# Optimization experiments

Measured on AMD Instinct MI355X. Metric: run time of the kernel, lower is better.

## Reference

```python
import jax, jax.numpy as jnp
import numpy as np

N_NODES = 200000
N_EDGES = 6400000
N_GRAPHS = 1000


def setup_inputs() -> dict:
    key = jax.random.key(0)
    ks = jax.random.split(key, 8)
    x = jax.random.normal(ks[0], (N_NODES, 2), dtype=jnp.float32)
    edge_index = jax.random.randint(ks[1], (2, N_EDGES), 0, N_NODES, dtype=jnp.int32)
    batch = jnp.sort(jax.random.randint(ks[2], (N_NODES,), 0, N_GRAPHS, dtype=jnp.int32))
    W1 = jax.random.normal(ks[3], (2, 16), dtype=jnp.float32) * (1.0 / np.sqrt(2))
    b1 = jnp.zeros((16,), jnp.float32)
    W2 = jax.random.normal(ks[4], (16, 32), dtype=jnp.float32) * (1.0 / np.sqrt(16))
    b2 = jnp.zeros((32,), jnp.float32)
    Wfc1 = jax.random.normal(ks[5], (32, 16), dtype=jnp.float32) * (1.0 / np.sqrt(32))
    bfc1 = jnp.zeros((16,), jnp.float32)
    Wfc2 = jax.random.normal(ks[6], (16, 1), dtype=jnp.float32) * (1.0 / np.sqrt(16))
    bfc2 = jnp.zeros((1,), jnp.float32)
    return {"x": x, "edge_index": edge_index, "batch": batch,
            "W1": W1, "b1": b1, "W2": W2, "b2": b2,
            "Wfc1": Wfc1, "bfc1": bfc1, "Wfc2": Wfc2, "bfc2": bfc2}


def _gcn_norm(edge_index, n_nodes):
    # PyG GCNConv default: add self loops, symmetric normalization.
    loops = jnp.arange(n_nodes, dtype=edge_index.dtype)
    src = jnp.concatenate([edge_index[0], loops])  # message source (row)
    dst = jnp.concatenate([edge_index[1], loops])  # aggregation target (col)
    deg = jax.ops.segment_sum(jnp.ones_like(dst, jnp.float32), dst, num_segments=n_nodes)
    dinv = jnp.where(deg > 0, jax.lax.rsqrt(jnp.maximum(deg, 1.0)), 0.0)
    norm = dinv[src] * dinv[dst]  # [E + N]
    return src, dst, norm


def _gcn_conv(h, W, b, src, dst, norm, n_nodes):
    h = h @ W                                      # transform first (small width)
    msg = h[src] * norm[:, None]                   # gather + scale: [E+N, F]
    out = jax.ops.segment_sum(msg, dst, num_segments=n_nodes)
    return out + b


def reference(x, edge_index, batch, W1, b1, W2, b2, Wfc1, bfc1, Wfc2, bfc2):
    n = x.shape[0]
    src, dst, norm = _gcn_norm(edge_index, n)
    h = jax.nn.relu(_gcn_conv(x, W1, b1, src, dst, norm, n))
    h = jax.nn.relu(_gcn_conv(h, W2, b2, src, dst, norm, n))
    # global_mean_pool over graph ids
    sums = jax.ops.segment_sum(h, batch, num_segments=N_GRAPHS)
    cnts = jax.ops.segment_sum(jnp.ones((n,), h.dtype), batch, num_segments=N_GRAPHS)
    pooled = sums / jnp.maximum(cnts, 1.0)[:, None]  # [G, 32]
    out = jax.nn.relu(pooled @ Wfc1 + bfc1)
    out = out @ Wfc2 + bfc2                          # [G, 1]
    return out.squeeze(-1)
```

## Files before the change

kernel.cpp:

```cpp
#include <hip/hip_runtime.h>
#include <hip/hip_fp16.h>

static inline size_t align256(size_t x) { return (x + 255) & ~size_t(255); }

#define CAP 36864

__global__ __launch_bounds__(512) void k_scatter(const int* __restrict__ ei,
                                                 int* __restrict__ bcursor,
                                                 unsigned* __restrict__ bdata, int E) {
    __shared__ int lcount[256];
    __shared__ int gbase[256];
    int t = threadIdx.x;
    if (t < 256) lcount[t] = 0;
    __syncthreads();
    int chunk = blockIdx.x * 8192;
    int srcv[16], bkt[16], rank[16], dl[16];
#pragma unroll
    for (int k = 0; k < 16; ++k) {
        int e = chunk + k * 512 + t;
        bkt[k] = -1;
        if (e < E) {
            int sv = ei[e], d = ei[E + e];
            int b = d >> 10;
            srcv[k] = sv; bkt[k] = b; dl[k] = d & 1023;
            rank[k] = atomicAdd(&lcount[b], 1);
        }
    }
    __syncthreads();
    if (t < 256) {
        int c = lcount[t];
        gbase[t] = t * CAP + (c ? atomicAdd(&bcursor[t], c) : 0);
    }
    __syncthreads();
#pragma unroll
    for (int k = 0; k < 16; ++k) {
        if (bkt[k] >= 0)
            bdata[gbase[bkt[k]] + rank[k]] = ((unsigned)dl[k] << 18) | (unsigned)srcv[k];
    }
}

__global__ void k_bscan2(const int* __restrict__ bcursor, int* __restrict__ bbase,
                         int NBv, int E) {
    __shared__ int lds[256];
    int t = threadIdx.x;
    int v = (t < NBv) ? bcursor[t] : 0;
    lds[t] = v;
    __syncthreads();
    for (int off = 1; off < 256; off <<= 1) {
        int x = (t >= off) ? lds[t - off] : 0;
        __syncthreads();
        lds[t] += x;
        __syncthreads();
    }
    if (t < NBv) bbase[t] = lds[t] - v;
    if (t == 0) bbase[NBv] = E;
}

__global__ __launch_bounds__(1024) void k_build(const unsigned* __restrict__ bdata,
                                                const int* __restrict__ bbase,
                                                int* __restrict__ row_ptr,
                                                float* __restrict__ dinv,
                                                int* __restrict__ col,
                                                const float* __restrict__ x,
                                                float2* __restrict__ xt,
                                                int N, int E, int NBv) {
    __shared__ int curs[1024];
    __shared__ int sums[256];
    __shared__ int stage[CAP];
    int* hist = stage;
    int bkt = blockIdx.x;
    int t = threadIdx.x;
    int tb = bbase[bkt];
    int count = bbase[bkt + 1] - tb;
    int fs = bkt * CAP;
    int node0 = bkt << 10;
    int nn = N - node0; if (nn > 1024) nn = 1024;
    hist[t] = 0;
    __syncthreads();
    for (int e = t; e < count; e += 1024)
        atomicAdd(&hist[bdata[fs + e] >> 18], 1);
    __syncthreads();
    int v0 = 0, v1 = 0, v2 = 0, v3 = 0, s = 0;
    if (t < 256) {
        int b4 = t * 4;
        v0 = hist[b4]; v1 = hist[b4 + 1]; v2 = hist[b4 + 2]; v3 = hist[b4 + 3];
        s = v0 + v1 + v2 + v3;
        sums[t] = s;
    }
    __syncthreads();
    for (int off = 1; off < 256; off <<= 1) {
        int xv = 0;
        if (t < 256 && t >= off) xv = sums[t - off];
        __syncthreads();
        if (t < 256) sums[t] += xv;
        __syncthreads();
    }
    if (t < 256) {
        int b4 = t * 4;
        int e0 = sums[t] - s;
        int e1 = e0 + v0, e2 = e1 + v1, e3 = e2 + v2;
        curs[b4] = e0; curs[b4 + 1] = e1; curs[b4 + 2] = e2; curs[b4 + 3] = e3;
        if (b4 < nn)     { row_ptr[node0 + b4]     = tb + e0; dinv[node0 + b4]     = rsqrtf((float)v0 + 1.f); }
        if (b4 + 1 < nn) { row_ptr[node0 + b4 + 1] = tb + e1; dinv[node0 + b4 + 1] = rsqrtf((float)v1 + 1.f); }
        if (b4 + 2 < nn) { row_ptr[node0 + b4 + 2] = tb + e2; dinv[node0 + b4 + 2] = rsqrtf((float)v2 + 1.f); }
        if (b4 + 3 < nn) { row_ptr[node0 + b4 + 3] = tb + e3; dinv[node0 + b4 + 3] = rsqrtf((float)v3 + 1.f); }
    }
    if (bkt == NBv - 1 && t == 0) row_ptr[N] = E;
    __syncthreads();
    for (int e = t; e < count; e += 1024) {
        unsigned p = bdata[fs + e];
        int dl = p >> 18;
        int pos = atomicAdd(&curs[dl], 1);
        stage[pos] = (int)(p & 0x3FFFFu);
    }
    __syncthreads();
    for (int i = t; i < count; i += 1024)
        col[tb + i] = stage[i];
    for (int i = t; i < nn; i += 1024) {
        int node = node0 + i;
        float d2 = dinv[node];
        xt[node] = make_float2(x[node * 2] * d2, x[node * 2 + 1] * d2);
    }
}

__global__ __launch_bounds__(256) void k_conv1_fused(const int* __restrict__ rp,
                                                     const int* __restrict__ col,
                                                     const float2* __restrict__ xt,
                                                     const float* __restrict__ dinv,
                                                     const float* __restrict__ W1,
                                                     const float* __restrict__ b1,
                                                     uint2* __restrict__ ht, int n) {
    int gt = blockIdx.x * 256 + threadIdx.x;
    int node = gt >> 2;
    int q = gt & 3;
    if (node >= n) return;
    int rs = rp[node], re = rp[node + 1];
    float a0 = 0.f, a1 = 0.f;
    int e = rs + q;
    for (; e + 12 < re; e += 16) {
        int c0 = __builtin_nontemporal_load(col + e);
        int c1 = __builtin_nontemporal_load(col + e + 4);
        int c2 = __builtin_nontemporal_load(col + e + 8);
        int c3 = __builtin_nontemporal_load(col + e + 12);
        float2 v0 = xt[c0];
        float2 v1 = xt[c1];
        float2 v2 = xt[c2];
        float2 v3 = xt[c3];
        a0 += (v0.x + v1.x) + (v2.x + v3.x);
        a1 += (v0.y + v1.y) + (v2.y + v3.y);
    }
    for (; e < re; e += 4) {
        float2 v = xt[__builtin_nontemporal_load(col + e)];
        a0 += v.x; a1 += v.y;
    }
    if (q == 0) { float2 sf = xt[node]; a0 += sf.x; a1 += sf.y; }
    a0 += __shfl_xor(a0, 1); a0 += __shfl_xor(a0, 2);
    a1 += __shfl_xor(a1, 1); a1 += __shfl_xor(a1, 2);
    float dv = dinv[node];
    a0 *= dv; a1 *= dv;
    int f0 = q * 4;
    float v0 = fmaxf(a0 * W1[f0]     + a1 * W1[16 + f0]     + b1[f0],     0.f) * dv;
    float v1 = fmaxf(a0 * W1[f0 + 1] + a1 * W1[16 + f0 + 1] + b1[f0 + 1], 0.f) * dv;
    float v2 = fmaxf(a0 * W1[f0 + 2] + a1 * W1[16 + f0 + 2] + b1[f0 + 2], 0.f) * dv;
    float v3 = fmaxf(a0 * W1[f0 + 3] + a1 * W1[16 + f0 + 3] + b1[f0 + 3], 0.f) * dv;
    __half2 h0 = __floats2half2_rn(v0, v1);
    __half2 h1 = __floats2half2_rn(v2, v3);
    uint2 w;
    w.x = *reinterpret_cast<unsigned*>(&h0);
    w.y = *reinterpret_cast<unsigned*>(&h1);
    ht[(size_t)node * 4 + q] = w;
}

__global__ __launch_bounds__(256) void k_gather2(const int* __restrict__ rp,
                                                 const int* __restrict__ col,
                                                 const uint4* __restrict__ ht,
                                                 const float* __restrict__ dinv,
                                                 float* __restrict__ agg, int N) {
    int gt = blockIdx.x * 256 + threadIdx.x;
    int node = gt >> 1;
    int hf = gt & 1;
    if (node >= N) return;
    int rs = rp[node], re = rp[node + 1];
    const uint4* __restrict__ base = ht + hf;
    float s0 = 0.f, s1 = 0.f, s2 = 0.f, s3 = 0.f, s4 = 0.f, s5 = 0.f, s6 = 0.f, s7 = 0.f;
    int e = rs;
    for (; e + 8 <= re; e += 8) {
        int c[8];
#pragma unroll
        for (int k = 0; k < 8; ++k) c[k] = __builtin_nontemporal_load(col + e + k);
        uint4 u[8];
#pragma unroll
        for (int k = 0; k < 8; ++k) u[k] = base[(size_t)c[k] * 2];
#pragma unroll
        for (int k = 0; k < 8; ++k) {
            float2 f0 = __half22float2(*reinterpret_cast<__half2*>(&u[k].x));
            float2 f1 = __half22float2(*reinterpret_cast<__half2*>(&u[k].y));
            float2 f2 = __half22float2(*reinterpret_cast<__half2*>(&u[k].z));
            float2 f3 = __half22float2(*reinterpret_cast<__half2*>(&u[k].w));
            s0 += f0.x; s1 += f0.y; s2 += f1.x; s3 += f1.y;
            s4 += f2.x; s5 += f2.y; s6 += f3.x; s7 += f3.y;
        }
    }
    for (; e < re; ++e) {
        uint4 u = base[(size_t)__builtin_nontemporal_load(col + e) * 2];
        float2 f0 = __half22float2(*reinterpret_cast<__half2*>(&u.x));
        float2 f1 = __half22float2(*reinterpret_cast<__half2*>(&u.y));
        float2 f2 = __half22float2(*reinterpret_cast<__half2*>(&u.z));
        float2 f3 = __half22float2(*reinterpret_cast<__half2*>(&u.w));
        s0 += f0.x; s1 += f0.y; s2 += f1.x; s3 += f1.y;
        s4 += f2.x; s5 += f2.y; s6 += f3.x; s7 += f3.y;
    }
    {
        uint4 u = base[(size_t)node * 2];
        float2 f0 = __half22float2(*reinterpret_cast<__half2*>(&u.x));
        float2 f1 = __half22float2(*reinterpret_cast<__half2*>(&u.y));
        float2 f2 = __half22float2(*reinterpret_cast<__half2*>(&u.z));
        float2 f3 = __half22float2(*reinterpret_cast<__half2*>(&u.w));
        s0 += f0.x; s1 += f0.y; s2 += f1.x; s3 += f1.y;
        s4 += f2.x; s5 += f2.y; s6 += f3.x; s7 += f3.y;
    }
    float dv = dinv[node];
    float* dst = agg + (size_t)node * 16 + hf * 8;
    __builtin_nontemporal_store(s0 * dv, dst);
    __builtin_nontemporal_store(s1 * dv, dst + 1);
    __builtin_nontemporal_store(s2 * dv, dst + 2);
    __builtin_nontemporal_store(s3 * dv, dst + 3);
    __builtin_nontemporal_store(s4 * dv, dst + 4);
    __builtin_nontemporal_store(s5 * dv, dst + 5);
    __builtin_nontemporal_store(s6 * dv, dst + 6);
    __builtin_nontemporal_store(s7 * dv, dst + 7);
}

__global__ __launch_bounds__(256) void k_trans_pool(const float* __restrict__ agg,
                                                    const float* __restrict__ W2,
                                                    const float* __restrict__ b2,
                                                    const int* __restrict__ batch,
                                                    float* __restrict__ gsum, int N) {
    __shared__ float aggs[64][17];
    __shared__ float h2s[64][33];
    __shared__ float w2s[512];
    __shared__ float b2s[32];
    __shared__ int   bids[64];
    int t = threadIdx.x;
    if (t < 128) ((float4*)w2s)[t] = ((const float4*)W2)[t];
    if (t < 32)  b2s[t] = b2[t];
    int node0 = blockIdx.x * 64;
    if (t < 64)  bids[t] = (node0 + t < N) ? batch[node0 + t] : -1;
    {
        int nl = t >> 2, q = t & 3;
        int node = node0 + nl;
        float4 v = make_float4(0.f, 0.f, 0.f, 0.f);
        if (node < N) v = *(const float4*)(agg + (size_t)node * 16 + (size_t)q * 4);
        int c0 = q * 4;
        aggs[nl][c0] = v.x; aggs[nl][c0 + 1] = v.y;
        aggs[nl][c0 + 2] = v.z; aggs[nl][c0 + 3] = v.w;
    }
    __syncthreads();
    {
        int nl = t >> 2;
        int jq = (t & 3) * 8;
        float o[8];
#pragma unroll
        for (int j = 0; j < 8; ++j) o[j] = b2s[jq + j];
#pragma unroll
        for (int k = 0; k < 16; ++k) {
            float a = aggs[nl][k];
#pragma unroll
            for (int j = 0; j < 8; ++j) o[j] += a * w2s[k * 32 + jq + j];
        }
#pragma unroll
        for (int j = 0; j < 8; ++j) h2s[nl][jq + j] = fmaxf(o[j], 0.f);
    }
    __syncthreads();
    if (t < 128) {
        int j = t & 31, seg = t >> 5;
        int nbeg = seg * 16, nend = nbeg + 16;
        float acc = 0.f;
        int cur = bids[nbeg];
        for (int n2 = nbeg; n2 < nend; ++n2) {
            int b = bids[n2];
            if (b != cur) {
                if (cur >= 0) atomicAdd(&gsum[(size_t)cur * 32 + j], acc);
                acc = 0.f; cur = b;
            }
            if (b >= 0) acc += h2s[n2][j];
        }
        if (cur >= 0) atomicAdd(&gsum[(size_t)cur * 32 + j], acc);
    }
}

__global__ void k_final(const float* __restrict__ gsum, const int* __restrict__ batch,
                        const float* __restrict__ Wfc1, const float* __restrict__ bfc1,
                        const float* __restrict__ Wfc2, const float* __restrict__ bfc2,
                        float* __restrict__ out, int G, int N) {
    int g = blockIdx.x * blockDim.x + threadIdx.x;
    if (g >= G) return;
    int lo = 0, hi = N;
    while (lo < hi) { int m = (lo + hi) >> 1; if (batch[m] < g) lo = m + 1; else hi = m; }
    int s = lo;
    lo = s; hi = N;
    while (lo < hi) { int m = (lo + hi) >> 1; if (batch[m] < g + 1) lo = m + 1; else hi = m; }
    float cnt = (float)(lo - s);
    float inv = 1.f / fmaxf(cnt, 1.f);
    float p[32];
#pragma unroll
    for (int i = 0; i < 32; ++i) p[i] = gsum[(size_t)g * 32 + i] * inv;
    float o = bfc2[0];
#pragma unroll
    for (int j = 0; j < 16; ++j) {
        float a = bfc1[j];
#pragma unroll
        for (int i = 0; i < 32; ++i) a += p[i] * Wfc1[i * 16 + j];
        o += fmaxf(a, 0.f) * Wfc2[j];
    }
    out[g] = o;
}

extern "C" void kernel_launch(void* const* d_in, const int* in_sizes, int n_in,
                              void* d_out, int out_size, void* d_ws, size_t ws_size,
                              hipStream_t stream) {
    const float* x     = (const float*)d_in[0];
    const int*   ei    = (const int*)d_in[1];
    const int*   batch = (const int*)d_in[2];
    const float* W1    = (const float*)d_in[3];
    const float* b1    = (const float*)d_in[4];
    const float* W2    = (const float*)d_in[5];
    const float* b2    = (const float*)d_in[6];
    const float* Wfc1  = (const float*)d_in[7];
    const float* bfc1  = (const float*)d_in[8];
    const float* Wfc2  = (const float*)d_in[9];
    const float* bfc2  = (const float*)d_in[10];
    float* out = (float*)d_out;

    const int N = in_sizes[0] / 2;
    const int E = in_sizes[1] / 2;
    const int G = out_size;
    const int NBv = (N + 1023) >> 10;

    char* ws = (char*)d_ws;
    size_t off = 0;
    float* dinv    = (float*)(ws + off); off += align256((size_t)N * 4);
    int*   row_ptr = (int*)(ws + off);   off += align256((size_t)(N + 1) * 4);
    int*   bcursor = (int*)(ws + off);   off += align256(256 * 4);
    int*   bbase   = (int*)(ws + off);   off += align256(257 * 4);
    float* gsum    = (float*)(ws + off); off += align256((size_t)G * 32 * 4);
    float2* xt     = (float2*)(ws + off); off += align256((size_t)N * 8);
    __half2* ht    = (__half2*)(ws + off); off += align256((size_t)N * 32);
    float* agg     = (float*)(ws + off); off += align256((size_t)N * 16 * 4);
    int*   col     = (int*)(ws + off);   off += align256((size_t)E * 4);
    unsigned* bdata = (unsigned*)(ws + off); off += align256((size_t)NBv * CAP * 4);

    const int BS = 256;

    hipMemsetAsync(bcursor, 0, 256 * 4, stream);
    hipMemsetAsync(gsum, 0, (size_t)G * 32 * 4, stream);

    k_scatter<<<(E + 8191) / 8192, 512, 0, stream>>>(ei, bcursor, bdata, E);
    k_bscan2<<<1, 256, 0, stream>>>(bcursor, bbase, NBv, E);
    k_build<<<NBv, 1024, 0, stream>>>(bdata, bbase, row_ptr, dinv, col, x, xt, N, E, NBv);

    k_conv1_fused<<<((size_t)N * 4 + 255) / 256, 256, 0, stream>>>(row_ptr, col, xt, dinv,
                                                                   W1, b1, (uint2*)ht, N);
    k_gather2<<<((size_t)N * 2 + 255) / 256, 256, 0, stream>>>(row_ptr, col, (const uint4*)ht,
                                                               dinv, agg, N);
    k_trans_pool<<<(N + 63) / 64, 256, 0, stream>>>(agg, W2, b2, batch, gsum, N);

    k_final<<<(G + BS - 1) / BS, BS, 0, stream>>>(gsum, batch, Wfc1, bfc1, Wfc2, bfc2,
                                                  out, G, N);
}
```

Measured before the change: 271.7 us.

## Split conv2 gather into two feature-half passes over separate fp16 tables

The conv1 output table is split into two arrays, each holding 8 of the 16 half-precision features per node (16 bytes per node). The neighbour gather then runs twice, once per half, with a deeper 16-wide unroll and 8-byte loads. Each pass touches a 3.2 MB table instead of 6.4 MB, so the randomly gathered rows are more likely to stay in cache. The cost is reading the column indices and row pointers twice and one extra kernel launch.

Result: slower. 335.0 us (+23.3%).

```diff
diff --git a/kernel.cpp b/kernel.cpp
--- a/kernel.cpp
+++ b/kernel.cpp
@@ -129,7 +129,8 @@
                                                      const float* __restrict__ dinv,
                                                      const float* __restrict__ W1,
                                                      const float* __restrict__ b1,
-                                                     uint2* __restrict__ ht, int n) {
+                                                     uint2* __restrict__ htA,
+                                                     uint2* __restrict__ htB, int n) {
     int gt = blockIdx.x * 256 + threadIdx.x;
     int node = gt >> 2;
     int q = gt & 3;
@@ -168,67 +169,55 @@
     uint2 w;
     w.x = *reinterpret_cast<unsigned*>(&h0);
     w.y = *reinterpret_cast<unsigned*>(&h1);
-    ht[(size_t)node * 4 + q] = w;
-}
-
-__global__ __launch_bounds__(256) void k_gather2(const int* __restrict__ rp,
-                                                 const int* __restrict__ col,
-                                                 const uint4* __restrict__ ht,
-                                                 const float* __restrict__ dinv,
-                                                 float* __restrict__ agg, int N) {
+    uint2* dst = (q < 2) ? htA : htB;
+    dst[(size_t)node * 2 + (q & 1)] = w;
+}
+
+__global__ __launch_bounds__(256) void k_gather2h(const int* __restrict__ rp,
+                                                  const int* __restrict__ col,
+                                                  const uint2* __restrict__ ht,
+                                                  const float* __restrict__ dinv,
+                                                  float* __restrict__ agg, int N, int half) {
     int gt = blockIdx.x * 256 + threadIdx.x;
     int node = gt >> 1;
     int hf = gt & 1;
     if (node >= N) return;
     int rs = rp[node], re = rp[node + 1];
-    const uint4* __restrict__ base = ht + hf;
-    float s0 = 0.f, s1 = 0.f, s2 = 0.f, s3 = 0.f, s4 = 0.f, s5 = 0.f, s6 = 0.f, s7 = 0.f;
+    const uint2* __restrict__ base = ht + hf;
+    float s0 = 0.f, s1 = 0.f, s2 = 0.f, s3 = 0.f;
     int e = rs;
-    for (; e + 8 <= re; e += 8) {
-        int c[8];
-#pragma unroll
-        for (int k = 0; k < 8; ++k) c[k] = __builtin_nontemporal_load(col + e + k);
-        uint4 u[8];
-#pragma unroll
-        for (int k = 0; k < 8; ++k) u[k] = base[(size_t)c[k] * 2];
-#pragma unroll
-        for (int k = 0; k < 8; ++k) {
+    for (; e + 16 <= re; e += 16) {
+        int c[16];
+#pragma unroll
+        for (int k = 0; k < 16; ++k) c[k] = __builtin_nontemporal_load(col + e + k);
+        uint2 u[16];
+#pragma unroll
+        for (int k = 0; k < 16; ++k) u[k] = base[(size_t)c[k] * 2];
+#pragma unroll
+        for (int k = 0; k < 16; ++k) {
             float2 f0 = __half22float2(*reinterpret_cast<__half2*>(&u[k].x));
             float2 f1 = __half22float2(*reinterpret_cast<__half2*>(&u[k].y));
-            float2 f2 = __half22float2(*reinterpret_cast<__half2*>(&u[k].z));
-            float2 f3 = __half22float2(*reinterpret_cast<__half2*>(&u[k].w));
             s0 += f0.x; s1 += f0.y; s2 += f1.x; s3 += f1.y;
-            s4 += f2.x; s5 += f2.y; s6 += f3.x; s7 += f3.y;
         }
     }
     for (; e < re; ++e) {
-        uint4 u = base[(size_t)__builtin_nontemporal_load(col + e) * 2];
+        uint2 u = base[(size_t)__builtin_nontemporal_load(col + e) * 2];
         float2 f0 = __half22float2(*reinterpret_cast<__half2*>(&u.x));
         float2 f1 = __half22float2(*reinterpret_cast<__half2*>(&u.y));
-        float2 f2 = __half22float2(*reinterpret_cast<__half2*>(&u.z));
-        float2 f3 = __half22float2(*reinterpret_cast<__half2*>(&u.w));
         s0 += f0.x; s1 += f0.y; s2 += f1.x; s3 += f1.y;
-        s4 += f2.x; s5 += f2.y; s6 += f3.x; s7 += f3.y;
     }
     {
-        uint4 u = base[(size_t)node * 2];
+        uint2 u = base[(size_t)node * 2];
         float2 f0 = __half22float2(*reinterpret_cast<__half2*>(&u.x));
         float2 f1 = __half22float2(*reinterpret_cast<__half2*>(&u.y));
-        float2 f2 = __half22float2(*reinterpret_cast<__half2*>(&u.z));
-        float2 f3 = __half22float2(*reinterpret_cast<__half2*>(&u.w));
         s0 += f0.x; s1 += f0.y; s2 += f1.x; s3 += f1.y;
-        s4 += f2.x; s5 += f2.y; s6 += f3.x; s7 += f3.y;
     }
     float dv = dinv[node];
-    float* dst = agg + (size_t)node * 16 + hf * 8;
+    float* dst = agg + (size_t)node * 16 + half * 8 + hf * 4;
     __builtin_nontemporal_store(s0 * dv, dst);
     __builtin_nontemporal_store(s1 * dv, dst + 1);
     __builtin_nontemporal_store(s2 * dv, dst + 2);
     __builtin_nontemporal_store(s3 * dv, dst + 3);
-    __builtin_nontemporal_store(s4 * dv, dst + 4);
-    __builtin_nontemporal_store(s5 * dv, dst + 5);
-    __builtin_nontemporal_store(s6 * dv, dst + 6);
-    __builtin_nontemporal_store(s7 * dv, dst + 7);
 }
 
 __global__ __launch_bounds__(256) void k_trans_pool(const float* __restrict__ agg,
@@ -345,7 +334,8 @@
     int*   bbase   = (int*)(ws + off);   off += align256(257 * 4);
     float* gsum    = (float*)(ws + off); off += align256((size_t)G * 32 * 4);
     float2* xt     = (float2*)(ws + off); off += align256((size_t)N * 8);
-    __half2* ht    = (__half2*)(ws + off); off += align256((size_t)N * 32);
+    uint2* htA     = (uint2*)(ws + off); off += align256((size_t)N * 16);
+    uint2* htB     = (uint2*)(ws + off); off += align256((size_t)N * 16);
     float* agg     = (float*)(ws + off); off += align256((size_t)N * 16 * 4);
     int*   col     = (int*)(ws + off);   off += align256((size_t)E * 4);
     unsigned* bdata = (unsigned*)(ws + off); off += align256((size_t)NBv * CAP * 4);
@@ -360,9 +350,11 @@
     k_build<<<NBv, 1024, 0, stream>>>(bdata, bbase, row_ptr, dinv, col, x, xt, N, E, NBv);
 
     k_conv1_fused<<<((size_t)N * 4 + 255) / 256, 256, 0, stream>>>(row_ptr, col, xt, dinv,
-                                                                   W1, b1, (uint2*)ht, N);
-    k_gather2<<<((size_t)N * 2 + 255) / 256, 256, 0, stream>>>(row_ptr, col, (const uint4*)ht,
-                                                               dinv, agg, N);
+                                                                   W1, b1, htA, htB, N);
+    k_gather2h<<<((size_t)N * 2 + 255) / 256, 256, 0, stream>>>(row_ptr, col, htA, dinv,
+                                                                agg, N, 0);
+    k_gather2h<<<((size_t)N * 2 + 255) / 256, 256, 0, stream>>>(row_ptr, col, htB, dinv,
+                                                                agg, N, 1);
     k_trans_pool<<<(N + 63) / 64, 256, 0, stream>>>(agg, W2, b2, batch, gsum, N);
 
     k_final<<<(G + BS - 1) / BS, BS, 0, stream>>>(gsum, batch, Wfc1, bfc1, Wfc2, bfc2,
```
